# Kernel tuning notes

Measured on AMD Instinct MI355X. Metric: run time of the kernel, lower is better.

## Reference

```python
import jax, jax.numpy as jnp
import numpy as np

WIN = 7            # skimage default win_size
K1 = 0.01
K2 = 0.03
DATA_RANGE = 1.0   # images are in [0, 1]
PAD = (WIN - 1) // 2


def _uniform_filter_valid(x):
    # x: [N, 1, H, W] -> valid 7x7 box filter (== skimage uniform_filter cropped by PAD)
    k = jnp.ones((1, 1, WIN, WIN), x.dtype) / (WIN * WIN)
    return jax.lax.conv_general_dilated(
        x, k, window_strides=(1, 1), padding='VALID',
        dimension_numbers=('NCHW', 'OIHW', 'NCHW'))


def _ssim_mean(a, b):
    # a, b: [B, C, H, W]; each [H, W] slice is one independent SSIM image
    B, C, H, W = a.shape
    x = a.reshape(B * C, 1, H, W)
    y = b.reshape(B * C, 1, H, W)

    ux = _uniform_filter_valid(x)
    uy = _uniform_filter_valid(y)
    uxx = _uniform_filter_valid(x * x)
    uyy = _uniform_filter_valid(y * y)
    uxy = _uniform_filter_valid(x * y)

    NP = WIN * WIN
    cov_norm = NP / (NP - 1.0)  # sample covariance correction (skimage default)
    vx = cov_norm * (uxx - ux * ux)
    vy = cov_norm * (uyy - uy * uy)
    vxy = cov_norm * (uxy - ux * uy)

    C1 = (K1 * DATA_RANGE) ** 2
    C2 = (K2 * DATA_RANGE) ** 2

    S = ((2.0 * ux * uy + C1) * (2.0 * vxy + C2)) / \
        ((ux * ux + uy * uy + C1) * (vx + vy + C2))

    # skimage crops PAD border then means; VALID conv already cropped it.
    # All images are the same size, so np.average(per-image means) == global mean.
    return jnp.mean(S)


def setup_inputs() -> dict:
    key = jax.random.key(0)
    k1, k2 = jax.random.split(key)
    pred = jax.random.uniform(k1, (32, 4, 384, 384), dtype=jnp.float32)
    actual = jax.random.uniform(k2, (32, 4, 384, 384), dtype=jnp.float32)
    return {"pred": pred, "actual": actual}


def reference(pred, actual):
    return _ssim_mean(pred, actual)
```

## Files before the change

### kernel.cpp

```cpp
#include <hip/hip_runtime.h>

#define WIN 7
#define OUT_W 126
#define OUT_H 16
#define IN_W 132
#define IN_H 22
#define RSTR 17
#define H 384
#define W 384
#define OH 378
#define OW 378
#define NIMG 128
#define TX 3
#define TY 24
#define NBLK (TX * TY * NIMG)

__device__ __forceinline__ float wave_reduce(float v) {
#pragma unroll
    for (int off = 32; off > 0; off >>= 1) v += __shfl_down(v, off, 64);
    return v;
}

__global__ __launch_bounds__(256) void ssim_main(const float* __restrict__ pred,
                                                 const float* __restrict__ act,
                                                 float* __restrict__ partials) {
    __shared__ float cs_sx[IN_W * RSTR];
    __shared__ float cs_sy[IN_W * RSTR];
    __shared__ float cs_sxx[IN_W * RSTR];
    __shared__ float cs_syy[IN_W * RSTR];
    __shared__ float cs_sxy[IN_W * RSTR];
    __shared__ float red[4];

    const int t = threadIdx.x;
    const int img = blockIdx.z;
    const int x0 = blockIdx.x * OUT_W;
    const int y0 = blockIdx.y * OUT_H;
    const size_t base = (size_t)img * H * W;
    const float* xp = pred + base;
    const float* yp = act + base;

    if (t < IN_W) {
        const int col = x0 + t;
        float xv[IN_H], yv[IN_H];
#pragma unroll
        for (int i = 0; i < IN_H; ++i) {
            const int row = y0 + i;
            const bool ok = row < H;
            xv[i] = ok ? xp[(size_t)row * W + col] : 0.f;
            yv[i] = ok ? yp[(size_t)row * W + col] : 0.f;
        }
        float sx = 0.f, sy = 0.f, sxx = 0.f, syy = 0.f, sxy = 0.f;
#pragma unroll
        for (int k = 0; k < WIN; ++k) {
            sx += xv[k];
            sy += yv[k];
            sxx = fmaf(xv[k], xv[k], sxx);
            syy = fmaf(yv[k], yv[k], syy);
            sxy = fmaf(xv[k], yv[k], sxy);
        }
        const int a = t * RSTR;
        cs_sx[a] = sx; cs_sy[a] = sy; cs_sxx[a] = sxx; cs_syy[a] = syy; cs_sxy[a] = sxy;
#pragma unroll
        for (int r = 1; r < OUT_H; ++r) {
            const float xn = xv[r + 6], yn = yv[r + 6];
            const float xo = xv[r - 1], yo = yv[r - 1];
            sx += xn - xo;
            sy += yn - yo;
            sxx = fmaf(xn, xn, fmaf(-xo, xo, sxx));
            syy = fmaf(yn, yn, fmaf(-yo, yo, syy));
            sxy = fmaf(xn, yn, fmaf(-xo, yo, sxy));
            cs_sx[a + r] = sx; cs_sy[a + r] = sy; cs_sxx[a + r] = sxx;
            cs_syy[a + r] = syy; cs_sxy[a + r] = sxy;
        }
    }
    __syncthreads();

    const int r = t & 15;
    const int g = t >> 4;
    const int c0 = g * 8;
    const int orow = y0 + r;

    const float INV = 1.0f / 49.0f;
    const float CN = 49.0f / 48.0f;
    const float C1f = 0.01f * 0.01f;
    const float C2f = 0.03f * 0.03f;

    float accS = 0.f;
    if (orow < OH) {
        float sx = 0.f, sy = 0.f, sxx = 0.f, syy = 0.f, sxy = 0.f;
#pragma unroll
        for (int k = 0; k < WIN - 1; ++k) {
            const int a = (c0 + k) * RSTR + r;
            sx += cs_sx[a]; sy += cs_sy[a]; sxx += cs_sxx[a];
            syy += cs_syy[a]; sxy += cs_sxy[a];
        }
#pragma unroll
        for (int k = 0; k < 8; ++k) {
            const int j = c0 + k;
            if (j < OUT_W) {
                const int an = (j + 6) * RSTR + r;
                sx += cs_sx[an]; sy += cs_sy[an]; sxx += cs_sxx[an];
                syy += cs_syy[an]; sxy += cs_sxy[an];

                const float ux = sx * INV, uy = sy * INV;
                const float uxx = sxx * INV, uyy = syy * INV, uxy = sxy * INV;
                const float ux2 = ux * ux, uy2 = uy * uy, uxuy = ux * uy;
                const float vx = CN * (uxx - ux2);
                const float vy = CN * (uyy - uy2);
                const float vxy = CN * (uxy - uxuy);
                const float num = fmaf(2.f, uxuy, C1f) * fmaf(2.f, vxy, C2f);
                const float den = (ux2 + uy2 + C1f) * (vx + vy + C2f);
                accS += num / den;

                const int ao = j * RSTR + r;
                sx -= cs_sx[ao]; sy -= cs_sy[ao]; sxx -= cs_sxx[ao];
                syy -= cs_syy[ao]; sxy -= cs_sxy[ao];
            }
        }
    }

    const float wsum = wave_reduce(accS);
    if ((t & 63) == 0) red[t >> 6] = wsum;
    __syncthreads();
    if (t == 0) {
        const float bsum = red[0] + red[1] + red[2] + red[3];
        partials[blockIdx.x + TX * (blockIdx.y + TY * blockIdx.z)] = bsum;
    }
}

__global__ __launch_bounds__(256) void ssim_finalize(const float* __restrict__ partials,
                                                     float* __restrict__ out) {
    __shared__ double red[256];
    const int t = threadIdx.x;
    double s = 0.0;
    for (int i = t; i < NBLK; i += 256) s += (double)partials[i];
    red[t] = s;
    __syncthreads();
#pragma unroll
    for (int off = 128; off > 0; off >>= 1) {
        if (t < off) red[t] += red[t + off];
        __syncthreads();
    }
    if (t == 0) out[0] = (float)(red[0] / ((double)NIMG * OH * OW));
}

extern "C" void kernel_launch(void* const* d_in, const int* in_sizes, int n_in,
                              void* d_out, int out_size, void* d_ws, size_t ws_size,
                              hipStream_t stream) {
    const float* pred = (const float*)d_in[0];
    const float* act  = (const float*)d_in[1];
    float* partials = (float*)d_ws;
    dim3 grid(TX, TY, NIMG);
    ssim_main<<<grid, 256, 0, stream>>>(pred, act, partials);
    ssim_finalize<<<1, 256, 0, stream>>>(partials, (float*)d_out);
}
```

Measured before the change: 190.7 us.

## Transpose column-sum LDS layout, vectorize horizontal pass, simplify SSIM algebra

Stores the vertical column sums row-major with pitch 132, so each thread in the horizontal pass reads 16 contiguous values per statistic as float4 vectors instead of scalar strided loads. The SSIM formula is rewritten on raw window sums with rescaled constants, which drops the 1/49 scaling and replaces the divide with a fast reciprocal. Tile height shrinks to 15 rows (26 row tiles), finalize runs with 1024 threads, and launch bounds request 4 blocks per CU. In exchange, 16 of 256 threads sit idle in the horizontal pass, vertical halo overhead rises, and the approximate reciprocal may change precision slightly.

```diff
diff --git a/kernel.cpp b/kernel.cpp
--- a/kernel.cpp
+++ b/kernel.cpp
@@ -2,17 +2,18 @@
 
 #define WIN 7
 #define OUT_W 126
-#define OUT_H 16
+#define OUT_H 15
 #define IN_W 132
-#define IN_H 22
-#define RSTR 17
+#define IN_H 21
+#define PITCH 132
+#define AELEM (OUT_H * PITCH)
 #define H 384
 #define W 384
 #define OH 378
 #define OW 378
 #define NIMG 128
 #define TX 3
-#define TY 24
+#define TY 26
 #define NBLK (TX * TY * NIMG)
 
 __device__ __forceinline__ float wave_reduce(float v) {
@@ -21,14 +22,10 @@
     return v;
 }
 
-__global__ __launch_bounds__(256) void ssim_main(const float* __restrict__ pred,
-                                                 const float* __restrict__ act,
-                                                 float* __restrict__ partials) {
-    __shared__ float cs_sx[IN_W * RSTR];
-    __shared__ float cs_sy[IN_W * RSTR];
-    __shared__ float cs_sxx[IN_W * RSTR];
-    __shared__ float cs_syy[IN_W * RSTR];
-    __shared__ float cs_sxy[IN_W * RSTR];
+__global__ __launch_bounds__(256, 4) void ssim_main(const float* __restrict__ pred,
+                                                    const float* __restrict__ act,
+                                                    float* __restrict__ partials) {
+    __shared__ __align__(16) float cs[5 * AELEM + 16];
     __shared__ float red[4];
 
     const int t = threadIdx.x;
@@ -36,18 +33,18 @@
     const int x0 = blockIdx.x * OUT_W;
     const int y0 = blockIdx.y * OUT_H;
     const size_t base = (size_t)img * H * W;
-    const float* xp = pred + base;
-    const float* yp = act + base;
 
     if (t < IN_W) {
         const int col = x0 + t;
+        const float* xc = pred + base + col;
+        const float* yc = act + base + col;
         float xv[IN_H], yv[IN_H];
 #pragma unroll
         for (int i = 0; i < IN_H; ++i) {
             const int row = y0 + i;
             const bool ok = row < H;
-            xv[i] = ok ? xp[(size_t)row * W + col] : 0.f;
-            yv[i] = ok ? yp[(size_t)row * W + col] : 0.f;
+            xv[i] = ok ? xc[(size_t)row * W] : 0.f;
+            yv[i] = ok ? yc[(size_t)row * W] : 0.f;
         }
         float sx = 0.f, sy = 0.f, sxx = 0.f, syy = 0.f, sxy = 0.f;
 #pragma unroll
@@ -58,8 +55,11 @@
             syy = fmaf(yv[k], yv[k], syy);
             sxy = fmaf(xv[k], yv[k], sxy);
         }
-        const int a = t * RSTR;
-        cs_sx[a] = sx; cs_sy[a] = sy; cs_sxx[a] = sxx; cs_syy[a] = syy; cs_sxy[a] = sxy;
+        cs[0 * AELEM + t] = sx;
+        cs[1 * AELEM + t] = sy;
+        cs[2 * AELEM + t] = sxx;
+        cs[3 * AELEM + t] = syy;
+        cs[4 * AELEM + t] = sxy;
 #pragma unroll
         for (int r = 1; r < OUT_H; ++r) {
             const float xn = xv[r + 6], yn = yv[r + 6];
@@ -69,8 +69,12 @@
             sxx = fmaf(xn, xn, fmaf(-xo, xo, sxx));
             syy = fmaf(yn, yn, fmaf(-yo, yo, syy));
             sxy = fmaf(xn, yn, fmaf(-xo, yo, sxy));
-            cs_sx[a + r] = sx; cs_sy[a + r] = sy; cs_sxx[a + r] = sxx;
-            cs_syy[a + r] = syy; cs_sxy[a + r] = sxy;
+            const int a = r * PITCH + t;
+            cs[0 * AELEM + a] = sx;
+            cs[1 * AELEM + a] = sy;
+            cs[2 * AELEM + a] = sxx;
+            cs[3 * AELEM + a] = syy;
+            cs[4 * AELEM + a] = sxy;
         }
     }
     __syncthreads();
@@ -78,66 +82,66 @@
     const int r = t & 15;
     const int g = t >> 4;
     const int c0 = g * 8;
-    const int orow = y0 + r;
 
-    const float INV = 1.0f / 49.0f;
-    const float CN = 49.0f / 48.0f;
-    const float C1f = 0.01f * 0.01f;
-    const float C2f = 0.03f * 0.03f;
+    const float C1B = 0.2401f;
+    const float C2B = 2.1168f;
 
-    float accS = 0.f;
-    if (orow < OH) {
-        float sx = 0.f, sy = 0.f, sxx = 0.f, syy = 0.f, sxy = 0.f;
+    float acc = 0.f;
+    if (r < OUT_H && (y0 + r) < OH) {
+        float S[5][8];
 #pragma unroll
-        for (int k = 0; k < WIN - 1; ++k) {
-            const int a = (c0 + k) * RSTR + r;
-            sx += cs_sx[a]; sy += cs_sy[a]; sxx += cs_sxx[a];
-            syy += cs_syy[a]; sxy += cs_sxy[a];
+        for (int a = 0; a < 5; ++a) {
+            const float* bp = &cs[a * AELEM + r * PITCH + c0];
+            const float4 q0 = *(const float4*)(bp);
+            const float4 q1 = *(const float4*)(bp + 4);
+            const float4 q2 = *(const float4*)(bp + 8);
+            const float4 q3 = *(const float4*)(bp + 12);
+            const float v[16] = {q0.x, q0.y, q0.z, q0.w, q1.x, q1.y, q1.z, q1.w,
+                                 q2.x, q2.y, q2.z, q2.w, q3.x, q3.y, q3.z, q3.w};
+            float s = ((v[0] + v[1]) + (v[2] + v[3])) + ((v[4] + v[5]) + v[6]);
+            S[a][0] = s;
+#pragma unroll
+            for (int j = 1; j < 8; ++j) {
+                s += v[j + 6] - v[j - 1];
+                S[a][j] = s;
+            }
         }
+        const int nmax = OUT_W - c0;
 #pragma unroll
-        for (int k = 0; k < 8; ++k) {
-            const int j = c0 + k;
-            if (j < OUT_W) {
-                const int an = (j + 6) * RSTR + r;
-                sx += cs_sx[an]; sy += cs_sy[an]; sxx += cs_sxx[an];
-                syy += cs_syy[an]; sxy += cs_sxy[an];
-
-                const float ux = sx * INV, uy = sy * INV;
-                const float uxx = sxx * INV, uyy = syy * INV, uxy = sxy * INV;
-                const float ux2 = ux * ux, uy2 = uy * uy, uxuy = ux * uy;
-                const float vx = CN * (uxx - ux2);
-                const float vy = CN * (uyy - uy2);
-                const float vxy = CN * (uxy - uxuy);
-                const float num = fmaf(2.f, uxuy, C1f) * fmaf(2.f, vxy, C2f);
-                const float den = (ux2 + uy2 + C1f) * (vx + vy + C2f);
-                accS += num / den;
-
-                const int ao = j * RSTR + r;
-                sx -= cs_sx[ao]; sy -= cs_sy[ao]; sxx -= cs_sxx[ao];
-                syy -= cs_syy[ao]; sxy -= cs_sxy[ao];
+        for (int j = 0; j < 8; ++j) {
+            if (j < nmax) {
+                const float Sx = S[0][j], Sy = S[1][j];
+                const float Sxx = S[2][j], Syy = S[3][j], Sxy = S[4][j];
+                const float p = Sx * Sy;
+                const float q = fmaf(Sx, Sx, Sy * Sy);
+                const float n1 = fmaf(2.f, p, C1B);
+                const float n2 = fmaf(98.f, Sxy, fmaf(-2.f, p, C2B));
+                const float d1 = q + C1B;
+                const float d2 = fmaf(49.f, Sxx + Syy, C2B - q);
+                acc = fmaf(n1 * n2, __builtin_amdgcn_rcpf(d1 * d2), acc);
             }
         }
     }
 
-    const float wsum = wave_reduce(accS);
+    const float wsum = wave_reduce(acc);
     if ((t & 63) == 0) red[t >> 6] = wsum;
     __syncthreads();
     if (t == 0) {
-        const float bsum = red[0] + red[1] + red[2] + red[3];
-        partials[blockIdx.x + TX * (blockIdx.y + TY * blockIdx.z)] = bsum;
+        partials[blockIdx.x + TX * (blockIdx.y + TY * blockIdx.z)] =
+            red[0] + red[1] + red[2] + red[3];
     }
 }
 
-__global__ __launch_bounds__(256) void ssim_finalize(const float* __restrict__ partials,
-                                                     float* __restrict__ out) {
-    __shared__ double red[256];
+__global__ __launch_bounds__(1024) void ssim_finalize(const float* __restrict__ partials,
+                                                      float* __restrict__ out) {
+    __shared__ double red[1024];
     const int t = threadIdx.x;
     double s = 0.0;
-    for (int i = t; i < NBLK; i += 256) s += (double)partials[i];
+    for (int i = t; i < NBLK; i += 1024) s += (double)partials[i];
     red[t] = s;
     __syncthreads();
 #pragma unroll
-    for (int off = 128; off > 0; off >>= 1) {
+    for (int off = 512; off > 0; off >>= 1) {
         if (t < off) red[t] += red[t + off];
         __syncthreads();
     }
@@ -152,5 +156,5 @@
     float* partials = (float*)d_ws;
     dim3 grid(TX, TY, NIMG);
     ssim_main<<<grid, 256, 0, stream>>>(pred, act, partials);
-    ssim_finalize<<<1, 256, 0, stream>>>(partials, (float*)d_out);
+    ssim_finalize<<<1, 1024, 0, stream>>>(partials, (float*)d_out);
 }
```

Measured after the change: 170.0 us. -10.9%, faster.
